# Optimization experiments

Measured on AMD Instinct MI355X. Metric: run time of the kernel, lower is better.

Reference implementation:

```python
import jax, jax.numpy as jnp
import numpy as np
from jax.scipy.special import logsumexp

B = 4096        # batch_size
D = 512         # feature dim
C = 128         # class_num
TEMP_F = 0.5
TEMP_L = 1.0
LAMBDA1 = 0.5
LAMBDA2 = 0.5
COS_EPS = 1e-8  # torch CosineSimilarity eps


def setup_inputs() -> dict:
    key = jax.random.key(0)
    k1, k2, k3, k4, k5 = jax.random.split(key, 5)
    return {
        "h1": jax.random.normal(k1, (B, D), dtype=jnp.float32),
        "h2": jax.random.normal(k2, (B, D), dtype=jnp.float32),
        "q1": jax.random.uniform(k3, (B, C), dtype=jnp.float32),
        "q2": jax.random.uniform(k4, (B, C), dtype=jnp.float32),
        "confidence": jax.random.uniform(k5, (B,), dtype=jnp.float32),
    }


def _ntxent_from_sim(sim, half):
    """NT-Xent per-row loss given full sim matrix [2*half, 2*half].

    Key identity: logits row r = [pos_r, negatives_r] where negatives exclude
    cols {r, partner(r)} and pos_r = sim[r, partner(r)]. Hence
    CE(logits, 0) = logsumexp over row excluding only the diagonal, minus pos.
    """
    N = 2 * half
    pos = jnp.concatenate([jnp.diagonal(sim, offset=half),
                           jnp.diagonal(sim, offset=-half)], axis=0)  # [N]
    eye = jnp.eye(N, dtype=bool)
    sim_masked = jnp.where(eye, -jnp.inf, sim)
    lse = logsumexp(sim_masked, axis=1)  # [N]
    return lse - pos  # per-row CE loss


def _forward_feature(h_i, h_j, confidence):
    b = h_i.shape[0]
    h = jnp.concatenate([h_i, h_j], axis=0)              # [2B, D]
    sim = jnp.matmul(h, h.T) / TEMP_F                     # [2B, 2B]
    loss = _ntxent_from_sim(sim, b)                       # [2B]
    loss = loss * jnp.tile(confidence, 2)                 # confidence.repeat(2)
    return loss.mean()


def _forward_label(q_i, q_j):
    c = q_i.shape[1]
    p_i = q_i.sum(0)
    p_i = p_i / p_i.sum()
    ne_i = jnp.log(jnp.float32(c)) + (p_i * jnp.log(p_i)).sum()
    p_j = q_j.sum(0)
    p_j = p_j / p_j.sum()
    ne_j = jnp.log(jnp.float32(c)) + (p_j * jnp.log(p_j)).sum()
    entropy = ne_i + ne_j

    q = jnp.concatenate([q_i.T, q_j.T], axis=0)           # [2C, B]
    norms = jnp.linalg.norm(q, axis=1)                    # [2C]
    denom = jnp.maximum(norms[:, None] * norms[None, :], COS_EPS)
    sim = (q @ q.T) / denom / TEMP_L                      # [2C, 2C]
    loss = _ntxent_from_sim(sim, c)                       # [2C]
    return loss.mean() + entropy


def reference(h1, h2, q1, q2, confidence):
    loss_feat = _forward_feature(h1, h2, confidence)
    loss_label = _forward_label(q1, q2)
    return LAMBDA1 * loss_feat + LAMBDA2 * loss_label
```

## Files before the change

### kernel.cpp

```cpp
#include <hip/hip_runtime.h>

typedef __attribute__((ext_vector_type(8))) short short8;
typedef __attribute__((ext_vector_type(4))) float f32x4;

#define NROW 8192
#define D_SZ 512

#define HB_OFF     0u
#define SPARTL_OFF 0u
#define SGRAM_OFF  4194304u
#define PSUMP_OFF  4456448u
#define FPART_OFF  4472832u
#define POS_OFF    8388608u
#define MPART_OFF  8421376u
#define SPARTF_OFF 8683520u

#define GLOAD_LDS(gp, lp)                                     \
  __builtin_amdgcn_global_load_lds(                           \
      (const __attribute__((address_space(1))) void*)(gp),    \
      (__attribute__((address_space(3))) void*)(lp), 16, 0, 0)

__device__ __forceinline__ unsigned short f32_to_bf16(float f) {
  unsigned int u = __float_as_uint(f);
  u = (u + 0x7FFFu + ((u >> 16) & 1u)) >> 16;
  return (unsigned short)u;
}

__global__ void convert_kernel(const float* __restrict__ h1, const float* __restrict__ h2,
                               unsigned short* __restrict__ hb) {
  int tid = blockIdx.x * 256 + threadIdx.x;
  float4 v = (tid < 524288) ? reinterpret_cast<const float4*>(h1)[tid]
                            : reinterpret_cast<const float4*>(h2)[tid - 524288];
  ushort4 o;
  o.x = f32_to_bf16(v.x); o.y = f32_to_bf16(v.y);
  o.z = f32_to_bf16(v.z); o.w = f32_to_bf16(v.w);
  reinterpret_cast<ushort4*>(hb)[tid] = o;
}

__global__ __launch_bounds__(512, 2) void feature_kernel(
    const short* __restrict__ hb, float* __restrict__ pos,
    float* __restrict__ mpart, float* __restrict__ spart) {
  __shared__ short lds_s[2][2][16384];
  const int tid = threadIdx.x;
  const int w = tid >> 6;
  const int lane = tid & 63;
  const int lo16 = lane & 15;
  const int grp = lane >> 4;
  const int lo7 = lo16 & 7;
  const int wr = w >> 2;
  const int wc = w & 3;
  const int cz = blockIdx.x;
  const int bt = blockIdx.y;
  const int R0 = bt * 256;
  const int CZ0 = cz * 1024;

  const int srow = tid >> 3;
  const int csrc = (tid & 7) ^ (srow & 7);
  const short* baseA = hb + (size_t)(R0 + srow) * D_SZ + csrc * 8;
  const short* baseB = hb + (size_t)(CZ0 + srow) * D_SZ + csrc * 8;

#define STAGE_STEP(ct_, bk_, buf_) do {                        \
    const short* sa_ = baseA + (bk_) * 64;                     \
    const short* sb_ = baseB + (ct_) * 131072 + (bk_) * 64;    \
    short* da_ = &lds_s[buf_][0][tid * 8];                     \
    short* db_ = &lds_s[buf_][1][tid * 8];                     \
    GLOAD_LDS(sa_, da_);                  GLOAD_LDS(sb_, db_);                  \
    GLOAD_LDS(sa_ + 32768, da_ + 4096);   GLOAD_LDS(sb_ + 32768, db_ + 4096);   \
    GLOAD_LDS(sa_ + 65536, da_ + 8192);   GLOAD_LDS(sb_ + 65536, db_ + 8192);   \
    GLOAD_LDS(sa_ + 98304, da_ + 12288);  GLOAD_LDS(sb_ + 98304, db_ + 12288);  \
  } while (0)

  float mrun[8], srun[8];
#pragma unroll
  for (int rf = 0; rf < 8; ++rf) { mrun[rf] = -INFINITY; srun[rf] = 0.f; }

  f32x4 acc[4][8];
#pragma unroll
  for (int cf = 0; cf < 4; ++cf)
#pragma unroll
    for (int rf = 0; rf < 8; ++rf) acc[cf][rf] = (f32x4){0, 0, 0, 0};

  const int rowbaseA = (wr * 128 + lo16) * 64;
  const int colbaseB = (wc * 64 + lo16) * 64;

  STAGE_STEP(0, 0, 0);
  __syncthreads();

#pragma unroll 1
  for (int step = 0; step < 32; ++step) {
    const int ct = step >> 3, bk = step & 7, buf = step & 1;
    if (step < 31) {
      const int s2 = step + 1;
      STAGE_STEP(s2 >> 3, s2 & 7, buf ^ 1);
    }
    const short* pA = &lds_s[buf][0][0];
    const short* pB = &lds_s[buf][1][0];

#pragma unroll
    for (int ksub = 0; ksub < 2; ++ksub) {
      const int chsw = ((ksub * 4 + grp) ^ lo7) * 8;
      short8 cf_[4], rf_[8];
#pragma unroll
      for (int cf = 0; cf < 4; ++cf)
        cf_[cf] = *reinterpret_cast<const short8*>(&pB[colbaseB + cf * 1024 + chsw]);
#pragma unroll
      for (int rf = 0; rf < 8; ++rf)
        rf_[rf] = *reinterpret_cast<const short8*>(&pA[rowbaseA + rf * 1024 + chsw]);
#pragma unroll
      for (int cf = 0; cf < 4; ++cf)
#pragma unroll
        for (int rf = 0; rf < 8; ++rf)
          acc[cf][rf] = __builtin_amdgcn_mfma_f32_16x16x32_bf16(cf_[cf], rf_[rf],
                                                                acc[cf][rf], 0, 0, 0);
    }

    if (bk == 7) {
      const int C0 = CZ0 + ct * 256;
      const bool hd = (C0 == R0);
      const bool hp = (C0 == ((R0 + 4096) & 8191));
#pragma unroll
      for (int rf = 0; rf < 8; ++rf) {
        const int row = R0 + wr * 128 + rf * 16 + lo16;
        float v[16];
#pragma unroll
        for (int cf = 0; cf < 4; ++cf)
#pragma unroll
          for (int j = 0; j < 4; ++j) v[cf * 4 + j] = acc[cf][rf][j] * 2.f;
        if (hd || hp) {
          const int prow = (row + 4096) & 8191;
#pragma unroll
          for (int cf = 0; cf < 4; ++cf)
#pragma unroll
            for (int j = 0; j < 4; ++j) {
              const int c = C0 + wc * 64 + cf * 16 + grp * 4 + j;
              if (hp && c == prow) pos[row] = v[cf * 4 + j];
              if (hd && c == row) v[cf * 4 + j] = -INFINITY;
            }
        }
        float tm = v[0];
#pragma unroll
        for (int i = 1; i < 16; ++i) tm = fmaxf(tm, v[i]);
        const float mn = fmaxf(mrun[rf], tm);
        float e = 0.f;
#pragma unroll
        for (int i = 0; i < 16; ++i) e += __expf(v[i] - mn);
        srun[rf] = srun[rf] * __expf(mrun[rf] - mn) + e;
        mrun[rf] = mn;
#pragma unroll
        for (int cf = 0; cf < 4; ++cf) acc[cf][rf] = (f32x4){0, 0, 0, 0};
      }
    }
    __syncthreads();
  }

#pragma unroll
  for (int rf = 0; rf < 8; ++rf) {
#pragma unroll
    for (int off = 16; off <= 32; off <<= 1) {
      float mo = __shfl_xor(mrun[rf], off), so = __shfl_xor(srun[rf], off);
      float mn = fmaxf(mrun[rf], mo);
      srun[rf] = srun[rf] * __expf(mrun[rf] - mn) + so * __expf(mo - mn);
      mrun[rf] = mn;
    }
  }

  float* marr = reinterpret_cast<float*>(&lds_s[0][0][0]);
  float* sarr = marr + 1024;
  if (grp == 0) {
#pragma unroll
    for (int rf = 0; rf < 8; ++rf) {
      const int idx = ((wr * 4 + wc) * 8 + rf) * 16 + lo16;
      marr[idx] = mrun[rf];
      sarr[idx] = srun[rf];
    }
  }
  __syncthreads();
  if (tid < 256) {
    const int row = tid;
    const int wr2 = row >> 7, rf2 = (row >> 4) & 7, lo2 = row & 15;
    float M = -INFINITY, S = 0.f;
#pragma unroll
    for (int wc2 = 0; wc2 < 4; ++wc2) {
      const int idx = ((wr2 * 4 + wc2) * 8 + rf2) * 16 + lo2;
      const float m = marr[idx], s = sarr[idx];
      const float mn = fmaxf(M, m);
      S = S * __expf(M - mn) + s * __expf(m - mn);
      M = mn;
    }
    mpart[cz * NROW + R0 + row] = M;
    spart[cz * NROW + R0 + row] = S;
  }
#undef STAGE_STEP
}

__global__ void combine_feature_kernel(const float* __restrict__ mpart,
                                       const float* __restrict__ spart,
                                       const float* __restrict__ pos,
                                       const float* __restrict__ conf,
                                       float* __restrict__ fpart) {
  __shared__ float red[256];
  int r = blockIdx.x * 256 + threadIdx.x;
  float M = -INFINITY;
#pragma unroll
  for (int k = 0; k < 8; ++k) M = fmaxf(M, mpart[k * NROW + r]);
  float S = 0.f;
#pragma unroll
  for (int k = 0; k < 8; ++k) S += spart[k * NROW + r] * __expf(mpart[k * NROW + r] - M);
  float lse = logf(S) + M;
  float loss = (lse - pos[r]) * conf[r & 4095];
  red[threadIdx.x] = loss;
  __syncthreads();
  for (int s = 128; s > 0; s >>= 1) {
    if (threadIdx.x < s) red[threadIdx.x] += red[threadIdx.x + s];
    __syncthreads();
  }
  if (threadIdx.x == 0) fpart[blockIdx.x] = red[0];
}

__global__ __launch_bounds__(256) void label_gemm_kernel(const float* __restrict__ q1,
                                                         const float* __restrict__ q2,
                                                         float* __restrict__ Spart) {
  __shared__ float As[32 * 64];
  __shared__ float Bs[32 * 64];
  const int t = threadIdx.x;
  const int kz = blockIdx.x >> 4;
  const int bi = (blockIdx.x >> 2) & 3;
  const int bj = blockIdx.x & 3;
  const int tx = t & 15, ty = t >> 4;
  float a[4][4];
#pragma unroll
  for (int dr = 0; dr < 4; ++dr)
#pragma unroll
    for (int dc = 0; dc < 4; ++dc) a[dr][dc] = 0.f;

  for (int ch = 0; ch < 8; ++ch) {
    const int kbase = kz * 256 + ch * 32;
    __syncthreads();
#pragma unroll
    for (int i = 0; i < 8; ++i) {
      int e = i * 256 + t;
      int kr = e >> 6, j = e & 63;
      int ca = bi * 64 + j;
      int cb = bj * 64 + j;
      As[kr * 64 + j] = (ca < 128) ? q1[(kbase + kr) * 128 + ca]
                                   : q2[(kbase + kr) * 128 + ca - 128];
      Bs[kr * 64 + j] = (cb < 128) ? q1[(kbase + kr) * 128 + cb]
                                   : q2[(kbase + kr) * 128 + cb - 128];
    }
    __syncthreads();
#pragma unroll 8
    for (int k = 0; k < 32; ++k) {
      float4 Av = *reinterpret_cast<const float4*>(&As[k * 64 + ty * 4]);
      float4 Bv = *reinterpret_cast<const float4*>(&Bs[k * 64 + tx * 4]);
      a[0][0] += Av.x * Bv.x; a[0][1] += Av.x * Bv.y; a[0][2] += Av.x * Bv.z; a[0][3] += Av.x * Bv.w;
      a[1][0] += Av.y * Bv.x; a[1][1] += Av.y * Bv.y; a[1][2] += Av.y * Bv.z; a[1][3] += Av.y * Bv.w;
      a[2][0] += Av.z * Bv.x; a[2][1] += Av.z * Bv.y; a[2][2] += Av.z * Bv.z; a[2][3] += Av.z * Bv.w;
      a[3][0] += Av.w * Bv.x; a[3][1] += Av.w * Bv.y; a[3][2] += Av.w * Bv.z; a[3][3] += Av.w * Bv.w;
    }
  }
  float* outp = Spart + (size_t)kz * 65536;
#pragma unroll
  for (int dr = 0; dr < 4; ++dr) {
    int r = bi * 64 + ty * 4 + dr;
    int c = bj * 64 + tx * 4;
    float4 o = {a[dr][0], a[dr][1], a[dr][2], a[dr][3]};
    *reinterpret_cast<float4*>(&outp[r * 256 + c]) = o;
  }
}

__global__ void label_prep_kernel(const float* __restrict__ q1, const float* __restrict__ q2,
                                  const float* __restrict__ Spart, float* __restrict__ S,
                                  float* __restrict__ psum_part) {
  const int b = blockIdx.x, t = threadIdx.x;
  if (b < 256) {
    int e = b * 256 + t;
    float acc = 0.f;
#pragma unroll
    for (int kz = 0; kz < 16; ++kz) acc += Spart[(size_t)kz * 65536 + e];
    S[e] = acc;
  } else {
    __shared__ float sd[256];
    int idx = b - 256;
    const float* q = (idx < 16) ? q1 : q2;
    int col = t & 127, rh = t >> 7;
    int rbase = (idx & 15) * 256 + rh;
    float acc = 0.f;
    for (int i = 0; i < 128; ++i) acc += q[(rbase + 2 * i) * 128 + col];
    sd[t] = acc;
    __syncthreads();
    if (t < 128) psum_part[idx * 128 + col] = sd[t] + sd[t + 128];
  }
}

__global__ __launch_bounds__(256) void label_final_kernel(
    const float* __restrict__ S, const float* __restrict__ psum_part,
    const float* __restrict__ fpart, float* __restrict__ out) {
  __shared__ float nrm[256], red[256], redl[256];
  __shared__ float entropy_sh, feat_sh;
  const int t = threadIdx.x;
  nrm[t] = sqrtf(fmaxf(S[t * 257], 0.f));
  const float* pp = psum_part + (t >> 7) * 2048 + (t & 127);
  float v = 0.f;
#pragma unroll
  for (int i = 0; i < 16; ++i) v += pp[i * 128];
  red[t] = v;
  redl[t] = v * logf(fmaxf(v, 1e-30f));
  __syncthreads();
  for (int s = 64; s > 0; s >>= 1) {
    if ((t & 127) < s) { red[t] += red[t + s]; redl[t] += redl[t + s]; }
    __syncthreads();
  }
  if (t == 0) {
    float tot1 = red[0], tot2 = red[128];
    float ne1 = logf(128.f) + (redl[0] / tot1 - logf(tot1));
    float ne2 = logf(128.f) + (redl[128] / tot2 - logf(tot2));
    entropy_sh = ne1 + ne2;
  }
  __syncthreads();
  red[t] = (t < 32) ? fpart[t] : 0.f;
  __syncthreads();
  for (int s = 128; s > 0; s >>= 1) {
    if (t < s) red[t] += red[t + s];
    __syncthreads();
  }
  if (t == 0) feat_sh = red[0];
  __syncthreads();

  const float nr = nrm[t];
  const float* Srow = S + t * 256;
  const int partner = (t + 128) & 255;
  float m = -INFINITY;
  for (int c = 0; c < 256; ++c) {
    if (c == t) continue;
    float sv = Srow[c] / fmaxf(nr * nrm[c], 1e-8f);
    m = fmaxf(m, sv);
  }
  float ssum = 0.f, posv = 0.f;
  for (int c = 0; c < 256; ++c) {
    float sv = Srow[c] / fmaxf(nr * nrm[c], 1e-8f);
    if (c == partner) posv = sv;
    if (c != t) ssum += __expf(sv - m);
  }
  float loss_r = (logf(ssum) + m) - posv;
  __syncthreads();
  red[t] = loss_r;
  __syncthreads();
  for (int s = 128; s > 0; s >>= 1) {
    if (t < s) red[t] += red[t + s];
    __syncthreads();
  }
  if (t == 0)
    out[0] = 0.5f * (feat_sh / 8192.f) + 0.5f * (red[0] / 256.f + entropy_sh);
}

extern "C" void kernel_launch(void* const* d_in, const int* in_sizes, int n_in,
                              void* d_out, int out_size, void* d_ws, size_t ws_size,
                              hipStream_t stream) {
  const float* h1 = (const float*)d_in[0];
  const float* h2 = (const float*)d_in[1];
  const float* q1 = (const float*)d_in[2];
  const float* q2 = (const float*)d_in[3];
  const float* conf = (const float*)d_in[4];
  float* out = (float*)d_out;
  char* ws = (char*)d_ws;

  unsigned short* hb = (unsigned short*)(ws + HB_OFF);
  float* pos    = (float*)(ws + POS_OFF);
  float* mpart  = (float*)(ws + MPART_OFF);
  float* spartf = (float*)(ws + SPARTF_OFF);
  float* SpartL = (float*)(ws + SPARTL_OFF);
  float* Sgram  = (float*)(ws + SGRAM_OFF);
  float* psump  = (float*)(ws + PSUMP_OFF);
  float* fpart  = (float*)(ws + FPART_OFF);

  convert_kernel<<<4096, 256, 0, stream>>>(h1, h2, hb);
  feature_kernel<<<dim3(8, 32), 512, 0, stream>>>((const short*)hb, pos, mpart, spartf);
  combine_feature_kernel<<<32, 256, 0, stream>>>(mpart, spartf, pos, conf, fpart);
  label_gemm_kernel<<<256, 256, 0, stream>>>(q1, q2, SpartL);
  label_prep_kernel<<<288, 256, 0, stream>>>(q1, q2, SpartL, Sgram, psump);
  label_final_kernel<<<1, 256, 0, stream>>>(Sgram, psump, fpart, out);
}
```

Baseline: 220.6 us.

## Compute positives in separate FP32 kernel and use partial vmcnt waits with raw barriers

```diff
diff --git a/kernel.cpp b/kernel.cpp
--- a/kernel.cpp
+++ b/kernel.cpp
@@ -37,8 +37,25 @@
   reinterpret_cast<ushort4*>(hb)[tid] = o;
 }
 
+__global__ void pos_kernel(const float* __restrict__ h1, const float* __restrict__ h2,
+                           float* __restrict__ pos) {
+  const int row = blockIdx.x * 4 + (threadIdx.x >> 6);
+  const int lane = threadIdx.x & 63;
+  const float4* a = reinterpret_cast<const float4*>(h1 + (size_t)row * D_SZ) + lane * 2;
+  const float4* b = reinterpret_cast<const float4*>(h2 + (size_t)row * D_SZ) + lane * 2;
+  float4 a0 = a[0], a1 = a[1], b0 = b[0], b1 = b[1];
+  float d = a0.x * b0.x + a0.y * b0.y + a0.z * b0.z + a0.w * b0.w +
+            a1.x * b1.x + a1.y * b1.y + a1.z * b1.z + a1.w * b1.w;
+#pragma unroll
+  for (int off = 1; off < 64; off <<= 1) d += __shfl_xor(d, off);
+  if (lane == 0) {
+    pos[row] = 2.f * d;
+    pos[row + 4096] = 2.f * d;
+  }
+}
+
 __global__ __launch_bounds__(512, 2) void feature_kernel(
-    const short* __restrict__ hb, float* __restrict__ pos,
+    const short* __restrict__ hb,
     float* __restrict__ mpart, float* __restrict__ spart) {
   __shared__ short lds_s[2][2][16384];
   const int tid = threadIdx.x;
@@ -84,7 +101,6 @@
   const int colbaseB = (wc * 64 + lo16) * 64;
 
   STAGE_STEP(0, 0, 0);
-  __syncthreads();
 
 #pragma unroll 1
   for (int step = 0; step < 32; ++step) {
@@ -92,7 +108,13 @@
     if (step < 31) {
       const int s2 = step + 1;
       STAGE_STEP(s2 >> 3, s2 & 7, buf ^ 1);
-    }
+      asm volatile("s_waitcnt vmcnt(8)" ::: "memory");
+    } else {
+      asm volatile("s_waitcnt vmcnt(0)" ::: "memory");
+    }
+    __builtin_amdgcn_s_barrier();
+    __builtin_amdgcn_sched_barrier(0);
+
     const short* pA = &lds_s[buf][0][0];
     const short* pB = &lds_s[buf][1][0];
 
@@ -117,7 +139,6 @@
     if (bk == 7) {
       const int C0 = CZ0 + ct * 256;
       const bool hd = (C0 == R0);
-      const bool hp = (C0 == ((R0 + 4096) & 8191));
 #pragma unroll
       for (int rf = 0; rf < 8; ++rf) {
         const int row = R0 + wr * 128 + rf * 16 + lo16;
@@ -126,15 +147,13 @@
         for (int cf = 0; cf < 4; ++cf)
 #pragma unroll
           for (int j = 0; j < 4; ++j) v[cf * 4 + j] = acc[cf][rf][j] * 2.f;
-        if (hd || hp) {
-          const int prow = (row + 4096) & 8191;
+        if (hd) {
 #pragma unroll
           for (int cf = 0; cf < 4; ++cf)
 #pragma unroll
             for (int j = 0; j < 4; ++j) {
               const int c = C0 + wc * 64 + cf * 16 + grp * 4 + j;
-              if (hp && c == prow) pos[row] = v[cf * 4 + j];
-              if (hd && c == row) v[cf * 4 + j] = -INFINITY;
+              if (c == row) v[cf * 4 + j] = -INFINITY;
             }
         }
         float tm = v[0];
@@ -150,7 +169,8 @@
         for (int cf = 0; cf < 4; ++cf) acc[cf][rf] = (f32x4){0, 0, 0, 0};
       }
     }
-    __syncthreads();
+    __builtin_amdgcn_sched_barrier(0);
+    __builtin_amdgcn_s_barrier();
   }
 
 #pragma unroll
@@ -374,7 +394,8 @@
   float* fpart  = (float*)(ws + FPART_OFF);
 
   convert_kernel<<<4096, 256, 0, stream>>>(h1, h2, hb);
-  feature_kernel<<<dim3(8, 32), 512, 0, stream>>>((const short*)hb, pos, mpart, spartf);
+  pos_kernel<<<1024, 256, 0, stream>>>(h1, h2, pos);
+  feature_kernel<<<dim3(8, 32), 512, 0, stream>>>((const short*)hb, mpart, spartf);
   combine_feature_kernel<<<32, 256, 0, stream>>>(mpart, spartf, pos, conf, fpart);
   label_gemm_kernel<<<256, 256, 0, stream>>>(q1, q2, SpartL);
   label_prep_kernel<<<288, 256, 0, stream>>>(q1, q2, SpartL, Sgram, psump);
```

Result: slower. 230.9 us (+4.7%).

## Exploit Gram symmetry: compute upper-triangle tiles, accumulate exp sums in double atomics

Applied to the files above, without the earlier changes.

```diff
diff --git a/kernel.cpp b/kernel.cpp
--- a/kernel.cpp
+++ b/kernel.cpp
@@ -9,11 +9,10 @@
 #define HB_OFF     0u
 #define SPARTL_OFF 0u
 #define SGRAM_OFF  4194304u
-#define PSUMP_OFF  4456448u
-#define FPART_OFF  4472832u
 #define POS_OFF    8388608u
-#define MPART_OFF  8421376u
-#define SPARTF_OFF 8683520u
+#define DSUM_OFF   8421376u
+#define PSUMP_OFF  8486912u
+#define FPART_OFF  8503296u
 
 #define GLOAD_LDS(gp, lp)                                     \
   __builtin_amdgcn_global_load_lds(                           \
@@ -26,20 +25,66 @@
   return (unsigned short)u;
 }
 
-__global__ void convert_kernel(const float* __restrict__ h1, const float* __restrict__ h2,
-                               unsigned short* __restrict__ hb) {
-  int tid = blockIdx.x * 256 + threadIdx.x;
-  float4 v = (tid < 524288) ? reinterpret_cast<const float4*>(h1)[tid]
-                            : reinterpret_cast<const float4*>(h2)[tid - 524288];
-  ushort4 o;
-  o.x = f32_to_bf16(v.x); o.y = f32_to_bf16(v.y);
-  o.z = f32_to_bf16(v.z); o.w = f32_to_bf16(v.w);
-  reinterpret_cast<ushort4*>(hb)[tid] = o;
+__device__ __forceinline__ double exp_pos(float x) {
+  if (x < -700.f) return 0.0;
+  float t = x * 1.44269504f;
+  float n = floorf(t);
+  double m = (double)exp2f(t - n);
+  int ni = (int)n;
+  double sc = __hiloint2double((1023 + ni) << 20, 0);
+  return m * sc;
+}
+
+__global__ void prep_kernel(const float* __restrict__ h1, const float* __restrict__ h2,
+                            const float* __restrict__ q1, const float* __restrict__ q2,
+                            unsigned short* __restrict__ hb, float* __restrict__ pos,
+                            double* __restrict__ dsum, float* __restrict__ psum_part) {
+  const int b = blockIdx.x, t = threadIdx.x;
+  if (b < 2048) {
+    __shared__ float dr_[4];
+    const int r0 = b * 2;
+    const int r = r0 + (t >> 7);
+    const int off4 = (t & 127) * 4;
+    float4 a = *reinterpret_cast<const float4*>(h1 + (size_t)r * D_SZ + off4);
+    float4 c = *reinterpret_cast<const float4*>(h2 + (size_t)r * D_SZ + off4);
+    ushort4 oa, oc;
+    oa.x = f32_to_bf16(a.x); oa.y = f32_to_bf16(a.y);
+    oa.z = f32_to_bf16(a.z); oa.w = f32_to_bf16(a.w);
+    oc.x = f32_to_bf16(c.x); oc.y = f32_to_bf16(c.y);
+    oc.z = f32_to_bf16(c.z); oc.w = f32_to_bf16(c.w);
+    *reinterpret_cast<ushort4*>(hb + (size_t)r * D_SZ + off4) = oa;
+    *reinterpret_cast<ushort4*>(hb + (size_t)(4096 + r) * D_SZ + off4) = oc;
+    float d = a.x * c.x + a.y * c.y + a.z * c.z + a.w * c.w;
+#pragma unroll
+    for (int off = 1; off < 64; off <<= 1) d += __shfl_xor(d, off);
+    if ((t & 63) == 0) dr_[t >> 6] = d;
+    __syncthreads();
+    if (t == 0) {
+      float v = 2.f * (dr_[0] + dr_[1]);
+      pos[r0] = v; pos[r0 + 4096] = v;
+    } else if (t == 128) {
+      float v = 2.f * (dr_[2] + dr_[3]);
+      pos[r0 + 1] = v; pos[r0 + 1 + 4096] = v;
+    }
+  } else if (b < 2080) {
+    __shared__ float sd[256];
+    int idx = b - 2048;
+    const float* q = (idx < 16) ? q1 : q2;
+    int col = t & 127, rh = t >> 7;
+    int rbase = (idx & 15) * 256 + rh;
+    float acc = 0.f;
+    for (int i = 0; i < 128; ++i) acc += q[(rbase + 2 * i) * 128 + col];
+    sd[t] = acc;
+    __syncthreads();
+    if (t < 128) psum_part[idx * 128 + col] = sd[t] + sd[t + 128];
+  } else {
+#pragma unroll
+    for (int k = 0; k < 32; ++k) dsum[t + 256 * k] = 0.0;
+  }
 }
 
 __global__ __launch_bounds__(512, 2) void feature_kernel(
-    const short* __restrict__ hb, float* __restrict__ pos,
-    float* __restrict__ mpart, float* __restrict__ spart) {
+    const short* __restrict__ hb, double* __restrict__ dsum) {
   __shared__ short lds_s[2][2][16384];
   const int tid = threadIdx.x;
   const int w = tid >> 6;
@@ -49,19 +94,22 @@
   const int lo7 = lo16 & 7;
   const int wr = w >> 2;
   const int wc = w & 3;
-  const int cz = blockIdx.x;
-  const int bt = blockIdx.y;
-  const int R0 = bt * 256;
-  const int CZ0 = cz * 1024;
+
+  int ti = 0, rem = blockIdx.x;
+#pragma unroll 1
+  while (rem >= 32 - ti) { rem -= 32 - ti; ++ti; }
+  const int tj = ti + rem;
+  const int R0 = ti * 256, C0 = tj * 256;
+  const bool diag = (ti == tj);
 
   const int srow = tid >> 3;
   const int csrc = (tid & 7) ^ (srow & 7);
   const short* baseA = hb + (size_t)(R0 + srow) * D_SZ + csrc * 8;
-  const short* baseB = hb + (size_t)(CZ0 + srow) * D_SZ + csrc * 8;
-
-#define STAGE_STEP(ct_, bk_, buf_) do {                        \
+  const short* baseB = hb + (size_t)(C0 + srow) * D_SZ + csrc * 8;
+
+#define STAGE_STEP(bk_, buf_) do {                             \
     const short* sa_ = baseA + (bk_) * 64;                     \
-    const short* sb_ = baseB + (ct_) * 131072 + (bk_) * 64;    \
+    const short* sb_ = baseB + (bk_) * 64;                     \
     short* da_ = &lds_s[buf_][0][tid * 8];                     \
     short* db_ = &lds_s[buf_][1][tid * 8];                     \
     GLOAD_LDS(sa_, da_);                  GLOAD_LDS(sb_, db_);                  \
@@ -70,10 +118,6 @@
     GLOAD_LDS(sa_ + 98304, da_ + 12288);  GLOAD_LDS(sb_ + 98304, db_ + 12288);  \
   } while (0)
 
-  float mrun[8], srun[8];
-#pragma unroll
-  for (int rf = 0; rf < 8; ++rf) { mrun[rf] = -INFINITY; srun[rf] = 0.f; }
-
   f32x4 acc[4][8];
 #pragma unroll
   for (int cf = 0; cf < 4; ++cf)
@@ -83,19 +127,15 @@
   const int rowbaseA = (wr * 128 + lo16) * 64;
   const int colbaseB = (wc * 64 + lo16) * 64;
 
-  STAGE_STEP(0, 0, 0);
+  STAGE_STEP(0, 0);
   __syncthreads();
 
 #pragma unroll 1
-  for (int step = 0; step < 32; ++step) {
-    const int ct = step >> 3, bk = step & 7, buf = step & 1;
-    if (step < 31) {
-      const int s2 = step + 1;
-      STAGE_STEP(s2 >> 3, s2 & 7, buf ^ 1);
-    }
+  for (int bk = 0; bk < 8; ++bk) {
+    const int buf = bk & 1;
+    if (bk < 7) STAGE_STEP(bk + 1, buf ^ 1);
     const short* pA = &lds_s[buf][0][0];
     const short* pB = &lds_s[buf][1][0];
-
 #pragma unroll
     for (int ksub = 0; ksub < 2; ++ksub) {
       const int chsw = ((ksub * 4 + grp) ^ lo7) * 8;
@@ -113,100 +153,59 @@
           acc[cf][rf] = __builtin_amdgcn_mfma_f32_16x16x32_bf16(cf_[cf], rf_[rf],
                                                                 acc[cf][rf], 0, 0, 0);
     }
-
-    if (bk == 7) {
-      const int C0 = CZ0 + ct * 256;
-      const bool hd = (C0 == R0);
-      const bool hp = (C0 == ((R0 + 4096) & 8191));
-#pragma unroll
-      for (int rf = 0; rf < 8; ++rf) {
-        const int row = R0 + wr * 128 + rf * 16 + lo16;
-        float v[16];
-#pragma unroll
-        for (int cf = 0; cf < 4; ++cf)
-#pragma unroll
-          for (int j = 0; j < 4; ++j) v[cf * 4 + j] = acc[cf][rf][j] * 2.f;
-        if (hd || hp) {
-          const int prow = (row + 4096) & 8191;
-#pragma unroll
-          for (int cf = 0; cf < 4; ++cf)
-#pragma unroll
-            for (int j = 0; j < 4; ++j) {
-              const int c = C0 + wc * 64 + cf * 16 + grp * 4 + j;
-              if (hp && c == prow) pos[row] = v[cf * 4 + j];
-              if (hd && c == row) v[cf * 4 + j] = -INFINITY;
-            }
-        }
-        float tm = v[0];
-#pragma unroll
-        for (int i = 1; i < 16; ++i) tm = fmaxf(tm, v[i]);
-        const float mn = fmaxf(mrun[rf], tm);
-        float e = 0.f;
-#pragma unroll
-        for (int i = 0; i < 16; ++i) e += __expf(v[i] - mn);
-        srun[rf] = srun[rf] * __expf(mrun[rf] - mn) + e;
-        mrun[rf] = mn;
-#pragma unroll
-        for (int cf = 0; cf < 4; ++cf) acc[cf][rf] = (f32x4){0, 0, 0, 0};
+    __syncthreads();
+  }
+
+#pragma unroll
+  for (int rf = 0; rf < 8; ++rf) {
+    const int row = R0 + wr * 128 + rf * 16 + lo16;
+    double rsum = 0.0;
+#pragma unroll
+    for (int cf = 0; cf < 4; ++cf)
+#pragma unroll
+      for (int j = 0; j < 4; ++j) {
+        if (diag && (C0 + wc * 64 + cf * 16 + grp * 4 + j) == row) continue;
+        rsum += exp_pos(acc[cf][rf][j] * 2.f);
       }
-    }
-    __syncthreads();
-  }
-
-#pragma unroll
-  for (int rf = 0; rf < 8; ++rf) {
-#pragma unroll
-    for (int off = 16; off <= 32; off <<= 1) {
-      float mo = __shfl_xor(mrun[rf], off), so = __shfl_xor(srun[rf], off);
-      float mn = fmaxf(mrun[rf], mo);
-      srun[rf] = srun[rf] * __expf(mrun[rf] - mn) + so * __expf(mo - mn);
-      mrun[rf] = mn;
-    }
-  }
-
-  float* marr = reinterpret_cast<float*>(&lds_s[0][0][0]);
-  float* sarr = marr + 1024;
-  if (grp == 0) {
-#pragma unroll
-    for (int rf = 0; rf < 8; ++rf) {
-      const int idx = ((wr * 4 + wc) * 8 + rf) * 16 + lo16;
-      marr[idx] = mrun[rf];
-      sarr[idx] = srun[rf];
-    }
-  }
-  __syncthreads();
-  if (tid < 256) {
-    const int row = tid;
-    const int wr2 = row >> 7, rf2 = (row >> 4) & 7, lo2 = row & 15;
-    float M = -INFINITY, S = 0.f;
-#pragma unroll
-    for (int wc2 = 0; wc2 < 4; ++wc2) {
-      const int idx = ((wr2 * 4 + wc2) * 8 + rf2) * 16 + lo2;
-      const float m = marr[idx], s = sarr[idx];
-      const float mn = fmaxf(M, m);
-      S = S * __expf(M - mn) + s * __expf(m - mn);
-      M = mn;
-    }
-    mpart[cz * NROW + R0 + row] = M;
-    spart[cz * NROW + R0 + row] = S;
+    rsum += __shfl_xor(rsum, 16);
+    rsum += __shfl_xor(rsum, 32);
+    if (grp == 0) atomicAdd(&dsum[row], rsum);
+  }
+  if (!diag) {
+#pragma unroll 1
+    for (int half = 0; half < 2; ++half) {
+      double colp[8] = {0, 0, 0, 0, 0, 0, 0, 0};
+#pragma unroll
+      for (int rf = 0; rf < 8; ++rf)
+#pragma unroll
+        for (int k = 0; k < 8; ++k)
+          colp[k] += exp_pos(acc[half * 2 + (k >> 2)][rf][k & 3] * 2.f);
+#pragma unroll
+      for (int off = 1; off < 16; off <<= 1)
+#pragma unroll
+        for (int k = 0; k < 8; ++k) colp[k] += __shfl_xor(colp[k], off);
+      if (lo16 < 8) {
+        double myv = 0.0;
+#pragma unroll
+        for (int k = 0; k < 8; ++k) myv = (lo16 == k) ? colp[k] : myv;
+        const int c = C0 + wc * 64 + (half * 2 + (lo16 >> 2)) * 16 + grp * 4 + (lo16 & 3);
+        atomicAdd(&dsum[c], myv);
+      }
+    }
   }
 #undef STAGE_STEP
 }
 
-__global__ void combine_feature_kernel(const float* __restrict__ mpart,
-                                       const float* __restrict__ spart,
+__global__ void combine_feature_kernel(const double* __restrict__ dsum,
                                        const float* __restrict__ pos,
                                        const float* __restrict__ conf,
                                        float* __restrict__ fpart) {
   __shared__ float red[256];
   int r = blockIdx.x * 256 + threadIdx.x;
-  float M = -INFINITY;
-#pragma unroll
-  for (int k = 0; k < 8; ++k) M = fmaxf(M, mpart[k * NROW + r]);
-  float S = 0.f;
-#pragma unroll
-  for (int k = 0; k < 8; ++k) S += spart[k * NROW + r] * __expf(mpart[k * NROW + r] - M);
-  float lse = logf(S) + M;
+  double d = dsum[r];
+  int e2 = ((__double2hiint(d) >> 20) & 0x7ff) - 1023;
+  double mant = d * __hiloint2double((1023 - e2) << 20, 0);
+  float lse = logf((float)mant) + (float)e2 * 0.69314718f;
   float loss = (lse - pos[r]) * conf[r & 4095];
   red[threadIdx.x] = loss;
   __syncthreads();
@@ -268,28 +267,13 @@
   }
 }
 
-__global__ void label_prep_kernel(const float* __restrict__ q1, const float* __restrict__ q2,
-                                  const float* __restrict__ Spart, float* __restrict__ S,
-                                  float* __restrict__ psum_part) {
-  const int b = blockIdx.x, t = threadIdx.x;
-  if (b < 256) {
-    int e = b * 256 + t;
-    float acc = 0.f;
-#pragma unroll
-    for (int kz = 0; kz < 16; ++kz) acc += Spart[(size_t)kz * 65536 + e];
-    S[e] = acc;
-  } else {
-    __shared__ float sd[256];
-    int idx = b - 256;
-    const float* q = (idx < 16) ? q1 : q2;
-    int col = t & 127, rh = t >> 7;
-    int rbase = (idx & 15) * 256 + rh;
-    float acc = 0.f;
-    for (int i = 0; i < 128; ++i) acc += q[(rbase + 2 * i) * 128 + col];
-    sd[t] = acc;
-    __syncthreads();
-    if (t < 128) psum_part[idx * 128 + col] = sd[t] + sd[t + 128];
-  }
+__global__ void label_combine_kernel(const float* __restrict__ Spart,
+                                     float* __restrict__ S) {
+  int e = blockIdx.x * 256 + threadIdx.x;
+  float acc = 0.f;
+#pragma unroll
+  for (int kz = 0; kz < 16; ++kz) acc += Spart[(size_t)kz * 65536 + e];
+  S[e] = acc;
 }
 
 __global__ __launch_bounds__(256) void label_final_kernel(
@@ -366,17 +350,16 @@
 
   unsigned short* hb = (unsigned short*)(ws + HB_OFF);
   float* pos    = (float*)(ws + POS_OFF);
-  float* mpart  = (float*)(ws + MPART_OFF);
-  float* spartf = (float*)(ws + SPARTF_OFF);
+  double* dsum  = (double*)(ws + DSUM_OFF);
   float* SpartL = (float*)(ws + SPARTL_OFF);
   float* Sgram  = (float*)(ws + SGRAM_OFF);
   float* psump  = (float*)(ws + PSUMP_OFF);
   float* fpart  = (float*)(ws + FPART_OFF);
 
-  convert_kernel<<<4096, 256, 0, stream>>>(h1, h2, hb);
-  feature_kernel<<<dim3(8, 32), 512, 0, stream>>>((const short*)hb, pos, mpart, spartf);
-  combine_feature_kernel<<<32, 256, 0, stream>>>(mpart, spartf, pos, conf, fpart);
+  prep_kernel<<<2081, 256, 0, stream>>>(h1, h2, q1, q2, hb, pos, dsum, psump);
+  feature_kernel<<<528, 512, 0, stream>>>((const short*)hb, dsum);
+  combine_feature_kernel<<<32, 256, 0, stream>>>(dsum, pos, conf, fpart);
   label_gemm_kernel<<<256, 256, 0, stream>>>(q1, q2, SpartL);
-  label_prep_kernel<<<288, 256, 0, stream>>>(q1, q2, SpartL, Sgram, psump);
+  label_combine_kernel<<<256, 256, 0, stream>>>(SpartL, Sgram);
   label_final_kernel<<<1, 256, 0, stream>>>(Sgram, psump, fpart, out);
 }
```

Measured after the change: 480.1 us. 118% more time.
